# Optimization experiments

Measured on AMD Instinct MI355X. Metric: run time of the kernel, lower is better.

The kernel has to match this reference:

```python
import jax, jax.numpy as jnp
import numpy as np

EPSILON = 1e-19
MASKING_RATIO = 0.75
N_BINS = 64
SIGMA = 0.01


def setup_inputs() -> dict:
    key = jax.random.key(0)
    k1, k2 = jax.random.split(key)
    N, L, D = 4, 512, 1024
    P = 768  # 16*16*3 pixels per patch
    x = jax.random.normal(k1, (N, L, D), dtype=jnp.float32)
    img_pat = jax.random.uniform(k2, (N, L, P), dtype=jnp.float32)
    return {"x": x, "img_pat": img_pat}


def _entropy_kde(values, n_bins=N_BINS, sigma=SIGMA):
    # values: [N, L, P]; global min/max normalization as in the torch code
    bins = jnp.linspace(0.0, 1.0, n_bins, dtype=values.dtype)  # [B]
    vmin = values.min()
    vmax = values.max()
    nv = (values - vmin) / (vmax - vmin)
    # residuals: [N, L, B, P]
    resid = nv[:, :, None, :] - bins[None, None, :, None]
    kern = jnp.exp(-0.5 * (resid / sigma) ** 2)
    pdf = kern.mean(axis=3)  # [N, L, B]
    pdf = pdf / (pdf.sum(axis=2, keepdims=True) + EPSILON) + EPSILON
    return -jnp.sum(pdf * jnp.log(pdf), axis=-1)  # [N, L]


def reference(x, img_pat):
    # entropy_kde_masking branch of MaskingModule.forward
    N, L, D = x.shape
    len_keep = int(L * (1.0 - MASKING_RATIO))
    entropies = _entropy_kde(img_pat)                 # [N, L]
    ids_shuffle = jnp.argsort(entropies, axis=1)      # ascending (descending=False)
    ids_restore = jnp.argsort(ids_shuffle, axis=1)    # [N, L]
    ids_keep = ids_shuffle[:, :len_keep]              # [N, len_keep]
    x_masked = jnp.take_along_axis(x, ids_keep[:, :, None], axis=1)  # [N, len_keep, D]
    mask = jnp.ones((N, L), dtype=x.dtype).at[:, :len_keep].set(0.0)
    mask = jnp.take_along_axis(mask, ids_restore, axis=1)
    return (x_masked, mask, ids_restore)
```

## Files before the change

### kernel.cpp

```cpp
#include <hip/hip_runtime.h>

#define NB 4
#define LB 512
#define DB 1024
#define PB 768
#define NBINS 64
#define LEN_KEEP 128
#define EPSL 1e-19f
#define WIN 10

#if defined(__has_builtin)
#if __has_builtin(__builtin_amdgcn_exp2f)
#define HAVE_EXP2 1
#endif
#endif

__device__ __forceinline__ float fast_exp2(float x) {
#ifdef HAVE_EXP2
    return __builtin_amdgcn_exp2f(x);
#else
    return __expf(x * 0.69314718055994530942f);
#endif
}

__global__ void minmax_partial(const float4* __restrict__ v,
                               float* __restrict__ bmin, float* __restrict__ bmax) {
    __shared__ float smin[256], smax[256];
    int tid = threadIdx.x;
    int base = blockIdx.x * 256 + tid;
    float mn = 1e30f, mx = -1e30f;
#pragma unroll
    for (int k = 0; k < 6; ++k) {
        float4 t4 = v[base + k * 65536];
        mn = fminf(mn, fminf(fminf(t4.x, t4.y), fminf(t4.z, t4.w)));
        mx = fmaxf(mx, fmaxf(fmaxf(t4.x, t4.y), fmaxf(t4.z, t4.w)));
    }
    smin[tid] = mn; smax[tid] = mx;
    __syncthreads();
    for (int s = 128; s > 0; s >>= 1) {
        if (tid < s) {
            smin[tid] = fminf(smin[tid], smin[tid + s]);
            smax[tid] = fmaxf(smax[tid], smax[tid + s]);
        }
        __syncthreads();
    }
    if (tid == 0) { bmin[blockIdx.x] = smin[0]; bmax[blockIdx.x] = smax[0]; }
}

__global__ void entropy_kernel(const float* __restrict__ img,
                               const float* __restrict__ bmin,
                               const float* __restrict__ bmax,
                               float* __restrict__ ent) {
    __shared__ float sh[512];
    __shared__ float snv[PB];
    __shared__ int   cnt[NBINS];
    __shared__ int   bs[NBINS + 1];
    __shared__ int   pos[NBINS];

    int t = blockIdx.x;
    int tid = threadIdx.x;

    sh[tid] = bmin[tid]; sh[256 + tid] = bmax[tid];
    if (tid < NBINS) cnt[tid] = 0;
    __syncthreads();
    for (int s = 128; s > 0; s >>= 1) {
        if (tid < s) {
            sh[tid]       = fminf(sh[tid], sh[tid + s]);
            sh[256 + tid] = fmaxf(sh[256 + tid], sh[256 + tid + s]);
        }
        __syncthreads();
    }
    float vmin = sh[0], vmax = sh[256];
    float inv = 1.0f / (vmax - vmin);

    const float* row = img + (size_t)t * PB;
    float nv0 = (row[tid]       - vmin) * inv;
    float nv1 = (row[tid + 256] - vmin) * inv;
    float nv2 = (row[tid + 512] - vmin) * inv;
    int m0 = min(63, max(0, __float2int_rn(nv0 * 63.0f)));
    int m1 = min(63, max(0, __float2int_rn(nv1 * 63.0f)));
    int m2 = min(63, max(0, __float2int_rn(nv2 * 63.0f)));
    atomicAdd(&cnt[m0], 1);
    atomicAdd(&cnt[m1], 1);
    atomicAdd(&cnt[m2], 1);
    __syncthreads();

    if (tid < 64) {
        int c = cnt[tid];
        int incl = c;
        for (int off = 1; off < 64; off <<= 1) {
            int up = __shfl_up(incl, off, 64);
            if (tid >= off) incl += up;
        }
        bs[tid + 1] = incl;
        pos[tid] = incl - c;
        if (tid == 0) bs[0] = 0;
    }
    __syncthreads();

    snv[atomicAdd(&pos[m0], 1)] = nv0;
    snv[atomicAdd(&pos[m1], 1)] = nv1;
    snv[atomicAdd(&pos[m2], 1)] = nv2;
    __syncthreads();

    int lane = tid & 63;
    int w = tid >> 6;
    float bv = (float)lane * (1.0f / 63.0f);
    int lo = bs[max(0, lane - WIN)];
    int hi = bs[min(NBINS, lane + WIN + 1)];
    const float negC = -7213.4755859375f;
    float acc = 0.0f;
    for (int j = lo + w; j < hi; j += 4) {
        float d = snv[j] - bv;
        acc += fast_exp2(d * d * negC);
    }
    sh[w * NBINS + lane] = acc;
    __syncthreads();

    if (tid < 64) {
        float pdf = (sh[lane] + sh[64 + lane] + sh[128 + lane] + sh[192 + lane])
                    * (1.0f / (float)PB);
        float s = pdf;
        for (int m = 1; m < 64; m <<= 1) s += __shfl_xor(s, m, 64);
        float p = pdf / (s + EPSL) + EPSL;
        float term = p * __logf(p);
        for (int m = 1; m < 64; m <<= 1) term += __shfl_xor(term, m, 64);
        if (tid == 0) ent[t] = -term;
    }
}

__global__ void rank_kernel(const float* __restrict__ ent,
                            int* __restrict__ ids_keep,
                            float* __restrict__ out_mask,
                            float* __restrict__ out_restore) {
    __shared__ float sh[LB];
    int e = blockIdx.x * 256 + threadIdx.x;
    int n = e >> 9;
    int i = e & 511;
    int tid = threadIdx.x;
    sh[tid]       = ent[n * LB + tid];
    sh[256 + tid] = ent[n * LB + 256 + tid];
    __syncthreads();

    unsigned long long ci =
        ((unsigned long long)__float_as_uint(sh[i & 255 | (i & 256)]) << 32) | (unsigned int)i;
    ci = ((unsigned long long)__float_as_uint(sh[i]) << 32) | (unsigned int)i;
    int r = 0;
#pragma unroll 8
    for (int j = 0; j < LB; ++j) {
        unsigned long long cj =
            ((unsigned long long)__float_as_uint(sh[j]) << 32) | (unsigned int)j;
        r += (cj < ci) ? 1 : 0;
    }
    out_restore[e] = (float)r;
    out_mask[e] = (r < LEN_KEEP) ? 0.0f : 1.0f;
    if (r < LEN_KEEP) ids_keep[n * LEN_KEEP + r] = i;
}

__global__ void gather_kernel(const float* __restrict__ x,
                              const int* __restrict__ ids_keep,
                              float* __restrict__ out) {
    int i = blockIdx.x;
    int n = blockIdx.y;
    int row = ids_keep[n * LEN_KEEP + i];
    const float4* src = (const float4*)(x + ((size_t)(n * LB + row)) * DB);
    float4* dst = (float4*)(out + ((size_t)(n * LEN_KEEP + i)) * DB);
    dst[threadIdx.x] = src[threadIdx.x];
}

extern "C" void kernel_launch(void* const* d_in, const int* in_sizes, int n_in,
                              void* d_out, int out_size, void* d_ws, size_t ws_size,
                              hipStream_t stream) {
    const float* x   = (const float*)d_in[0];
    const float* img = (const float*)d_in[1];

    float* out      = (float*)d_out;
    float* out_x    = out;
    float* out_mask = out + (size_t)NB * LEN_KEEP * DB;
    float* out_rest = out_mask + NB * LB;

    float* ws   = (float*)d_ws;
    float* bmin = ws;
    float* bmax = ws + 256;
    float* ent  = ws + 512;
    int*   ids  = (int*)(ws + 512 + NB * LB);

    minmax_partial<<<256, 256, 0, stream>>>((const float4*)img, bmin, bmax);
    entropy_kernel<<<NB * LB, 256, 0, stream>>>(img, bmin, bmax, ent);
    rank_kernel<<<8, 256, 0, stream>>>(ent, ids, out_mask, out_rest);
    gather_kernel<<<dim3(LEN_KEEP, NB), 256, 0, stream>>>(x, ids, out_x);
}
```

Baseline: 87.78 us.

## Fuse entropy, rank and gather into one cooperative kernel with grid barriers

Replaces three kernel launches (entropy, rank, gather) with a single cooperative kernel of 512 blocks. Each block now handles four rows, and a custom atomic grid barrier separates the entropy, ranking and gather phases. The KDE inner loop also reads sorted values as float4, so up to three extra values per window edge are summed (they add negligible mass). The aim is to cut launch gaps and per-block setup, such as the repeated min/max reduction, at the cost of spin-waiting barriers and idle blocks during the rank phase.

Result: slower. 161.9 us (+84.4%).

```diff
diff --git a/kernel.cpp b/kernel.cpp
--- a/kernel.cpp
+++ b/kernel.cpp
@@ -8,6 +8,7 @@
 #define LEN_KEEP 128
 #define EPSL 1e-19f
 #define WIN 10
+#define GRID2 512
 
 #if defined(__has_builtin)
 #if __has_builtin(__builtin_amdgcn_exp2f)
@@ -23,10 +24,32 @@
 #endif
 }
 
+__device__ __forceinline__ void grid_barrier(unsigned* cnt, unsigned* flag) {
+    __syncthreads();
+    if (threadIdx.x == 0) {
+        __threadfence();
+        unsigned old = __hip_atomic_fetch_add(cnt, 1u, __ATOMIC_ACQ_REL,
+                                              __HIP_MEMORY_SCOPE_AGENT);
+        if (old == GRID2 - 1) {
+            __hip_atomic_store(flag, 1u, __ATOMIC_RELEASE,
+                               __HIP_MEMORY_SCOPE_AGENT);
+        } else {
+            while (__hip_atomic_load(flag, __ATOMIC_RELAXED,
+                                     __HIP_MEMORY_SCOPE_AGENT) == 0u) {
+                __builtin_amdgcn_s_sleep(1);
+            }
+        }
+        __threadfence();
+    }
+    __syncthreads();
+}
+
 __global__ void minmax_partial(const float4* __restrict__ v,
-                               float* __restrict__ bmin, float* __restrict__ bmax) {
+                               float* __restrict__ bmin, float* __restrict__ bmax,
+                               unsigned* __restrict__ barr) {
     __shared__ float smin[256], smax[256];
     int tid = threadIdx.x;
+    if (blockIdx.x == 0 && tid < 4) barr[tid] = 0u;
     int base = blockIdx.x * 256 + tid;
     float mn = 1e30f, mx = -1e30f;
 #pragma unroll
@@ -47,21 +70,25 @@
     if (tid == 0) { bmin[blockIdx.x] = smin[0]; bmax[blockIdx.x] = smax[0]; }
 }
 
-__global__ void entropy_kernel(const float* __restrict__ img,
-                               const float* __restrict__ bmin,
-                               const float* __restrict__ bmax,
-                               float* __restrict__ ent) {
+__global__ __launch_bounds__(256, 2) void fused2(
+    const float* __restrict__ x, const float* __restrict__ img,
+    const float* __restrict__ bmin, const float* __restrict__ bmax,
+    float* __restrict__ out_x, float* __restrict__ out_mask,
+    float* __restrict__ out_rest, float* __restrict__ ws_ent,
+    int* __restrict__ ids, unsigned* __restrict__ barr)
+{
     __shared__ float sh[512];
-    __shared__ float snv[PB];
-    __shared__ int   cnt[NBINS];
-    __shared__ int   bs[NBINS + 1];
-    __shared__ int   pos[NBINS];
-
-    int t = blockIdx.x;
-    int tid = threadIdx.x;
+    __shared__ float4 snv4[PB / 4];
+    __shared__ int cnt[NBINS];
+    __shared__ int bs[NBINS + 1];
+    __shared__ int pos[NBINS];
+    float* snv = (float*)snv4;
+
+    int b = blockIdx.x, tid = threadIdx.x;
+    int lane = tid & 63;
+    int w = tid >> 6;
 
     sh[tid] = bmin[tid]; sh[256 + tid] = bmax[tid];
-    if (tid < NBINS) cnt[tid] = 0;
     __syncthreads();
     for (int s = 128; s > 0; s >>= 1) {
         if (tid < s) {
@@ -72,100 +99,104 @@
     }
     float vmin = sh[0], vmax = sh[256];
     float inv = 1.0f / (vmax - vmin);
-
-    const float* row = img + (size_t)t * PB;
-    float nv0 = (row[tid]       - vmin) * inv;
-    float nv1 = (row[tid + 256] - vmin) * inv;
-    float nv2 = (row[tid + 512] - vmin) * inv;
-    int m0 = min(63, max(0, __float2int_rn(nv0 * 63.0f)));
-    int m1 = min(63, max(0, __float2int_rn(nv1 * 63.0f)));
-    int m2 = min(63, max(0, __float2int_rn(nv2 * 63.0f)));
-    atomicAdd(&cnt[m0], 1);
-    atomicAdd(&cnt[m1], 1);
-    atomicAdd(&cnt[m2], 1);
-    __syncthreads();
-
-    if (tid < 64) {
-        int c = cnt[tid];
-        int incl = c;
-        for (int off = 1; off < 64; off <<= 1) {
-            int up = __shfl_up(incl, off, 64);
-            if (tid >= off) incl += up;
-        }
-        bs[tid + 1] = incl;
-        pos[tid] = incl - c;
-        if (tid == 0) bs[0] = 0;
-    }
-    __syncthreads();
-
-    snv[atomicAdd(&pos[m0], 1)] = nv0;
-    snv[atomicAdd(&pos[m1], 1)] = nv1;
-    snv[atomicAdd(&pos[m2], 1)] = nv2;
-    __syncthreads();
-
-    int lane = tid & 63;
-    int w = tid >> 6;
+    const float negC = -7213.4755859375f;
     float bv = (float)lane * (1.0f / 63.0f);
-    int lo = bs[max(0, lane - WIN)];
-    int hi = bs[min(NBINS, lane + WIN + 1)];
-    const float negC = -7213.4755859375f;
-    float acc = 0.0f;
-    for (int j = lo + w; j < hi; j += 4) {
-        float d = snv[j] - bv;
-        acc += fast_exp2(d * d * negC);
-    }
-    sh[w * NBINS + lane] = acc;
-    __syncthreads();
-
-    if (tid < 64) {
-        float pdf = (sh[lane] + sh[64 + lane] + sh[128 + lane] + sh[192 + lane])
-                    * (1.0f / (float)PB);
-        float s = pdf;
-        for (int m = 1; m < 64; m <<= 1) s += __shfl_xor(s, m, 64);
-        float p = pdf / (s + EPSL) + EPSL;
-        float term = p * __logf(p);
-        for (int m = 1; m < 64; m <<= 1) term += __shfl_xor(term, m, 64);
-        if (tid == 0) ent[t] = -term;
-    }
-}
-
-__global__ void rank_kernel(const float* __restrict__ ent,
-                            int* __restrict__ ids_keep,
-                            float* __restrict__ out_mask,
-                            float* __restrict__ out_restore) {
-    __shared__ float sh[LB];
-    int e = blockIdx.x * 256 + threadIdx.x;
-    int n = e >> 9;
-    int i = e & 511;
-    int tid = threadIdx.x;
-    sh[tid]       = ent[n * LB + tid];
-    sh[256 + tid] = ent[n * LB + 256 + tid];
-    __syncthreads();
-
-    unsigned long long ci =
-        ((unsigned long long)__float_as_uint(sh[i & 255 | (i & 256)]) << 32) | (unsigned int)i;
-    ci = ((unsigned long long)__float_as_uint(sh[i]) << 32) | (unsigned int)i;
-    int r = 0;
+
+    for (int u = 0; u < 4; ++u) {
+        int t = b * 4 + u;
+        __syncthreads();
+        if (tid < NBINS) cnt[tid] = 0;
+        __syncthreads();
+
+        const float* row = img + (size_t)t * PB;
+        float nv0 = (row[tid]       - vmin) * inv;
+        float nv1 = (row[tid + 256] - vmin) * inv;
+        float nv2 = (row[tid + 512] - vmin) * inv;
+        int m0 = min(63, max(0, __float2int_rn(nv0 * 63.0f)));
+        int m1 = min(63, max(0, __float2int_rn(nv1 * 63.0f)));
+        int m2 = min(63, max(0, __float2int_rn(nv2 * 63.0f)));
+        atomicAdd(&cnt[m0], 1);
+        atomicAdd(&cnt[m1], 1);
+        atomicAdd(&cnt[m2], 1);
+        __syncthreads();
+
+        if (tid < 64) {
+            int c = cnt[tid];
+            int incl = c;
+            for (int off = 1; off < 64; off <<= 1) {
+                int up = __shfl_up(incl, off, 64);
+                if (tid >= off) incl += up;
+            }
+            bs[tid + 1] = incl;
+            pos[tid] = incl - c;
+            if (tid == 0) bs[0] = 0;
+        }
+        __syncthreads();
+
+        snv[atomicAdd(&pos[m0], 1)] = nv0;
+        snv[atomicAdd(&pos[m1], 1)] = nv1;
+        snv[atomicAdd(&pos[m2], 1)] = nv2;
+        __syncthreads();
+
+        int c0 = bs[max(0, lane - WIN)] >> 2;
+        int c1 = (bs[min(NBINS, lane + WIN + 1)] + 3) >> 2;
+        float acc = 0.0f;
+        for (int c = c0 + w; c < c1; c += 4) {
+            float4 v = snv4[c];
+            float d0 = v.x - bv, d1 = v.y - bv, d2 = v.z - bv, d3 = v.w - bv;
+            acc += fast_exp2(d0 * d0 * negC);
+            acc += fast_exp2(d1 * d1 * negC);
+            acc += fast_exp2(d2 * d2 * negC);
+            acc += fast_exp2(d3 * d3 * negC);
+        }
+        sh[w * NBINS + lane] = acc;
+        __syncthreads();
+
+        if (tid < 64) {
+            float pdf = (sh[lane] + sh[64 + lane] + sh[128 + lane] + sh[192 + lane])
+                        * (1.0f / (float)PB);
+            float s = pdf;
+            for (int m = 1; m < 64; m <<= 1) s += __shfl_xor(s, m, 64);
+            float p = pdf / (s + EPSL) + EPSL;
+            float term = p * __logf(p);
+            for (int m = 1; m < 64; m <<= 1) term += __shfl_xor(term, m, 64);
+            if (tid == 0) ws_ent[t] = -term;
+        }
+    }
+
+    grid_barrier(barr + 0, barr + 1);
+
+    if (b < 8) {
+        int e = b * 256 + tid;
+        int n = e >> 9;
+        int i = e & 511;
+        sh[tid]       = ws_ent[n * LB + tid];
+        sh[256 + tid] = ws_ent[n * LB + 256 + tid];
+        __syncthreads();
+        unsigned long long ci =
+            ((unsigned long long)__float_as_uint(sh[i]) << 32) | (unsigned int)i;
+        int r = 0;
 #pragma unroll 8
-    for (int j = 0; j < LB; ++j) {
-        unsigned long long cj =
-            ((unsigned long long)__float_as_uint(sh[j]) << 32) | (unsigned int)j;
-        r += (cj < ci) ? 1 : 0;
-    }
-    out_restore[e] = (float)r;
-    out_mask[e] = (r < LEN_KEEP) ? 0.0f : 1.0f;
-    if (r < LEN_KEEP) ids_keep[n * LEN_KEEP + r] = i;
-}
-
-__global__ void gather_kernel(const float* __restrict__ x,
-                              const int* __restrict__ ids_keep,
-                              float* __restrict__ out) {
-    int i = blockIdx.x;
-    int n = blockIdx.y;
-    int row = ids_keep[n * LEN_KEEP + i];
-    const float4* src = (const float4*)(x + ((size_t)(n * LB + row)) * DB);
-    float4* dst = (float4*)(out + ((size_t)(n * LEN_KEEP + i)) * DB);
-    dst[threadIdx.x] = src[threadIdx.x];
+        for (int j = 0; j < LB; ++j) {
+            unsigned long long cj =
+                ((unsigned long long)__float_as_uint(sh[j]) << 32) | (unsigned int)j;
+            r += (cj < ci) ? 1 : 0;
+        }
+        out_rest[e] = (float)r;
+        out_mask[e] = (r < LEN_KEEP) ? 0.0f : 1.0f;
+        if (r < LEN_KEEP) ids[n * LEN_KEEP + r] = i;
+    }
+
+    grid_barrier(barr + 2, barr + 3);
+
+    {
+        int n = b >> 7;
+        int i = b & 127;
+        int row = ids[n * LEN_KEEP + i];
+        const float4* src = (const float4*)(x + ((size_t)(n * LB + row)) * DB);
+        float4* dst = (float4*)(out_x + ((size_t)b) * DB);
+        dst[tid] = src[tid];
+    }
 }
 
 extern "C" void kernel_launch(void* const* d_in, const int* in_sizes, int n_in,
@@ -179,14 +210,18 @@
     float* out_mask = out + (size_t)NB * LEN_KEEP * DB;
     float* out_rest = out_mask + NB * LB;
 
-    float* ws   = (float*)d_ws;
-    float* bmin = ws;
-    float* bmax = ws + 256;
-    float* ent  = ws + 512;
-    int*   ids  = (int*)(ws + 512 + NB * LB);
-
-    minmax_partial<<<256, 256, 0, stream>>>((const float4*)img, bmin, bmax);
-    entropy_kernel<<<NB * LB, 256, 0, stream>>>(img, bmin, bmax, ent);
-    rank_kernel<<<8, 256, 0, stream>>>(ent, ids, out_mask, out_rest);
-    gather_kernel<<<dim3(LEN_KEEP, NB), 256, 0, stream>>>(x, ids, out_x);
-}
+    float*    ws   = (float*)d_ws;
+    float*    bmin = ws;
+    float*    bmax = ws + 256;
+    float*    ent  = ws + 512;
+    int*      ids  = (int*)(ws + 512 + NB * LB);
+    unsigned* barr = (unsigned*)(ws + 512 + NB * LB + 512);
+
+    minmax_partial<<<256, 256, 0, stream>>>((const float4*)img, bmin, bmax, barr);
+
+    void* args[] = { (void*)&x, (void*)&img, (void*)&bmin, (void*)&bmax,
+                     (void*)&out_x, (void*)&out_mask, (void*)&out_rest,
+                     (void*)&ent, (void*)&ids, (void*)&barr };
+    hipLaunchCooperativeKernel((const void*)fused2, dim3(GRID2), dim3(256),
+                               args, 0, stream);
+}
```

## Shrink KDE window, cut partial min/max count, split rank work across lanes

Applied to the files above, without the earlier changes.

Reduces the min/max partial blocks from 256 to 64, so each entropy block can reduce the 64 partials with wave shuffles instead of a shared-memory tree with many barriers. Narrows the KDE bin window from 10 to 6 neighbouring bins, cutting exp evaluations per bin. The rank kernel now uses two threads per element, each scanning half the entries and combining counts with a shuffle, which doubles the block count. The narrower window drops kernel contributions from values farther than about 0.095 from a bin centre. Those contributions are negligible at sigma 0.01, but the result is still an approximation.

Measured after the change: 80.16 us. -8.7%, faster.

```diff
diff --git a/kernel.cpp b/kernel.cpp
--- a/kernel.cpp
+++ b/kernel.cpp
@@ -7,7 +7,7 @@
 #define NBINS 64
 #define LEN_KEEP 128
 #define EPSL 1e-19f
-#define WIN 10
+#define WIN 6
 
 #if defined(__has_builtin)
 #if __has_builtin(__builtin_amdgcn_exp2f)
@@ -30,8 +30,8 @@
     int base = blockIdx.x * 256 + tid;
     float mn = 1e30f, mx = -1e30f;
 #pragma unroll
-    for (int k = 0; k < 6; ++k) {
-        float4 t4 = v[base + k * 65536];
+    for (int k = 0; k < 24; ++k) {
+        float4 t4 = v[base + k * 16384];
         mn = fminf(mn, fminf(fminf(t4.x, t4.y), fminf(t4.z, t4.w)));
         mx = fmaxf(mx, fmaxf(fmaxf(t4.x, t4.y), fmaxf(t4.z, t4.w)));
     }
@@ -51,7 +51,7 @@
                                const float* __restrict__ bmin,
                                const float* __restrict__ bmax,
                                float* __restrict__ ent) {
-    __shared__ float sh[512];
+    __shared__ float sh[256];
     __shared__ float snv[PB];
     __shared__ int   cnt[NBINS];
     __shared__ int   bs[NBINS + 1];
@@ -59,18 +59,20 @@
 
     int t = blockIdx.x;
     int tid = threadIdx.x;
+    int lane = tid & 63;
+    int w = tid >> 6;
 
-    sh[tid] = bmin[tid]; sh[256 + tid] = bmax[tid];
     if (tid < NBINS) cnt[tid] = 0;
+    if (tid < 64) {
+        float mn = bmin[tid], mx = bmax[tid];
+        for (int m = 1; m < 64; m <<= 1) {
+            mn = fminf(mn, __shfl_xor(mn, m, 64));
+            mx = fmaxf(mx, __shfl_xor(mx, m, 64));
+        }
+        if (tid == 0) { sh[0] = mn; sh[1] = mx; }
+    }
     __syncthreads();
-    for (int s = 128; s > 0; s >>= 1) {
-        if (tid < s) {
-            sh[tid]       = fminf(sh[tid], sh[tid + s]);
-            sh[256 + tid] = fmaxf(sh[256 + tid], sh[256 + tid + s]);
-        }
-        __syncthreads();
-    }
-    float vmin = sh[0], vmax = sh[256];
+    float vmin = sh[0], vmax = sh[1];
     float inv = 1.0f / (vmax - vmin);
 
     const float* row = img + (size_t)t * PB;
@@ -103,8 +105,6 @@
     snv[atomicAdd(&pos[m2], 1)] = nv2;
     __syncthreads();
 
-    int lane = tid & 63;
-    int w = tid >> 6;
     float bv = (float)lane * (1.0f / 63.0f);
     int lo = bs[max(0, lane - WIN)];
     int hi = bs[min(NBINS, lane + WIN + 1)];
@@ -134,27 +134,31 @@
                             float* __restrict__ out_mask,
                             float* __restrict__ out_restore) {
     __shared__ float sh[LB];
-    int e = blockIdx.x * 256 + threadIdx.x;
-    int n = e >> 9;
-    int i = e & 511;
-    int tid = threadIdx.x;
+    int b = blockIdx.x, tid = threadIdx.x;
+    int n = b >> 2;
+    int i = (b & 3) * 128 + (tid >> 1);
+    int half = tid & 1;
+
     sh[tid]       = ent[n * LB + tid];
     sh[256 + tid] = ent[n * LB + 256 + tid];
     __syncthreads();
 
     unsigned long long ci =
-        ((unsigned long long)__float_as_uint(sh[i & 255 | (i & 256)]) << 32) | (unsigned int)i;
-    ci = ((unsigned long long)__float_as_uint(sh[i]) << 32) | (unsigned int)i;
+        ((unsigned long long)__float_as_uint(sh[i]) << 32) | (unsigned int)i;
     int r = 0;
+    int j0 = half * 256;
 #pragma unroll 8
-    for (int j = 0; j < LB; ++j) {
+    for (int j = j0; j < j0 + 256; ++j) {
         unsigned long long cj =
             ((unsigned long long)__float_as_uint(sh[j]) << 32) | (unsigned int)j;
         r += (cj < ci) ? 1 : 0;
     }
-    out_restore[e] = (float)r;
-    out_mask[e] = (r < LEN_KEEP) ? 0.0f : 1.0f;
-    if (r < LEN_KEEP) ids_keep[n * LEN_KEEP + r] = i;
+    r += __shfl_xor(r, 1, 64);
+    if (half == 0) {
+        out_restore[n * LB + i] = (float)r;
+        out_mask[n * LB + i] = (r < LEN_KEEP) ? 0.0f : 1.0f;
+        if (r < LEN_KEEP) ids_keep[n * LEN_KEEP + r] = i;
+    }
 }
 
 __global__ void gather_kernel(const float* __restrict__ x,
@@ -181,12 +185,12 @@
 
     float* ws   = (float*)d_ws;
     float* bmin = ws;
-    float* bmax = ws + 256;
-    float* ent  = ws + 512;
-    int*   ids  = (int*)(ws + 512 + NB * LB);
+    float* bmax = ws + 64;
+    float* ent  = ws + 128;
+    int*   ids  = (int*)(ws + 128 + NB * LB);
 
-    minmax_partial<<<256, 256, 0, stream>>>((const float4*)img, bmin, bmax);
+    minmax_partial<<<64, 256, 0, stream>>>((const float4*)img, bmin, bmax);
     entropy_kernel<<<NB * LB, 256, 0, stream>>>(img, bmin, bmax, ent);
-    rank_kernel<<<8, 256, 0, stream>>>(ent, ids, out_mask, out_rest);
+    rank_kernel<<<16, 256, 0, stream>>>(ent, ids, out_mask, out_rest);
     gather_kernel<<<dim3(LEN_KEEP, NB), 256, 0, stream>>>(x, ids, out_x);
 }
```
